# Kernel tuning notes

Measured on AMD Instinct MI355X. Metric: run time of the kernel, lower is better.

## Reference

```python
import jax, jax.numpy as jnp
import numpy as np

B, N, F_IN, F_HID, F_OUT = 16, 1024, 512, 512, 512


def setup_inputs() -> dict:
    key = jax.random.key(0)
    ks = jax.random.split(key, 8)
    return {
        "batch_graph": jax.random.normal(ks[0], (B, N, F_IN), dtype=jnp.float32),
        "adj": jax.random.uniform(ks[1], (B, N, N), dtype=jnp.float32),
        "W1": jax.random.normal(ks[2], (F_IN, F_HID), dtype=jnp.float32) * (1.0 / np.sqrt(F_IN)),
        "b1": jax.random.normal(ks[3], (F_HID,), dtype=jnp.float32) * 0.02,
        "W2": jax.random.normal(ks[4], (F_HID, F_HID), dtype=jnp.float32) * (1.0 / np.sqrt(F_HID)),
        "b2": jax.random.normal(ks[5], (F_HID,), dtype=jnp.float32) * 0.02,
        "W3": jax.random.normal(ks[6], (F_HID, F_OUT), dtype=jnp.float32) * (1.0 / np.sqrt(F_HID)),
        "b3": jax.random.normal(ks[7], (F_OUT,), dtype=jnp.float32) * 0.02,
    }


def _normalize_adj(adj):
    # torch: adj.sum(1) sums over rows -> per-column sums, shape [B, N]
    colsum = jnp.sum(adj, axis=1)
    r = jnp.where(colsum > 0, colsum ** -0.5, 0.0)  # inf -> 0 as in original
    # (adj @ diag(r)).T @ diag(r)  ==  r[:,None] * adj^T * r[None,:]  (per batch)
    return r[:, :, None] * jnp.swapaxes(adj, 1, 2) * r[:, None, :]


def reference(batch_graph, adj, W1, b1, W2, b2, W3, b3):
    # The original builds a dense (B*N)x(B*N) block-diagonal adjacency; the
    # block-diagonal matmul is mathematically a per-graph batched matmul.
    # Dropout is identity in eval mode.
    a = _normalize_adj(adj)  # [B, N, N]

    def layer(x, W, b):
        return jnp.einsum('bij,bjf->bif', a, x @ W) + b

    x = jax.nn.relu(layer(batch_graph, W1, b1))
    x = jax.nn.relu(layer(x, W2, b2))
    return layer(x, W3, b3)  # [B, N, F_OUT]
```

## Files before the change

### kernel.cpp

```cpp
#include <hip/hip_runtime.h>
#include <hip/hip_bf16.h>

typedef __bf16 bf16;
typedef __bf16 bf16x8 __attribute__((ext_vector_type(8)));
typedef float f32x4 __attribute__((ext_vector_type(4)));

#define B_ 16
#define N_ 1024
#define F_ 512

__device__ __forceinline__ float rdv(const void* p, size_t i, int f32) {
  return f32 ? ((const float*)p)[i] : (float)((const bf16*)p)[i];
}

__device__ __forceinline__ void gld16(const bf16* g, bf16* l) {
  __builtin_amdgcn_global_load_lds(
      (const __attribute__((address_space(1))) unsigned int*)g,
      (__attribute__((address_space(3))) unsigned int*)l, 16, 0, 0);
}

__global__ void k_detect(const unsigned* __restrict__ w, int* __restrict__ flag) {
  __shared__ int red[256];
  const int t = threadIdx.x;
  int c = 0;
  for (int i = t; i < 4096; i += 256) c += (((w[i] >> 7) & 0xFFu) >= 130u) ? 1 : 0;
  red[t] = c;
  __syncthreads();
  for (int s = 128; s > 0; s >>= 1) {
    if (t < s) red[t] += red[t + s];
    __syncthreads();
  }
  if (t == 0) flag[0] = (red[0] > 100) ? 1 : 0;
}

__global__ void k_prep(const void* b1, const void* b2, const void* b3,
                       const void* W1, const void* W2, const void* W3,
                       const void* X, const int* __restrict__ flag,
                       float* __restrict__ bc, bf16* __restrict__ Wt,
                       bf16* __restrict__ xc) {
  __shared__ float tile[32][33];
  const int bid = blockIdx.x;
  const int t = threadIdx.x;
  const int f = flag[0];
  if (bid < 6) {
    const int j = bid * 256 + t;
    const void* src = (j < 512) ? b1 : (j < 1024 ? b2 : b3);
    bc[j] = rdv(src, (size_t)(j & 511), f);
  } else if (bid < 774) {
    const int bid2 = bid - 6;
    const int z = bid2 >> 8, ti = bid2 & 255;
    const int f0 = (ti & 15) * 32, k0 = (ti >> 4) * 32;
    const int tx = t & 31, ty = t >> 5;
    const void* W = (z == 0) ? W1 : ((z == 1) ? W2 : W3);
    bf16* dst = Wt + (size_t)z * F_ * F_;
#pragma unroll
    for (int s = 0; s < 4; ++s)
      tile[ty + 8 * s][tx] = rdv(W, (size_t)(k0 + ty + 8 * s) * F_ + f0 + tx, f);
    __syncthreads();
#pragma unroll
    for (int s = 0; s < 4; ++s)
      dst[(size_t)(f0 + ty + 8 * s) * F_ + k0 + tx] = (bf16)tile[tx][ty + 8 * s];
  } else {
    const size_t i4 = ((size_t)(bid - 774) * 256 + t) * 4;
    if (f) {
      f32x4 v = *(const f32x4*)((const float*)X + i4);
      bf16 o[4] = {(bf16)v[0], (bf16)v[1], (bf16)v[2], (bf16)v[3]};
      *(ulong1*)&xc[i4] = *(ulong1*)o;
    } else {
      *(ulong1*)&xc[i4] = *(const ulong1*)((const bf16*)X + i4);
    }
  }
}

__global__ void k_colsum(const void* adj, const int* __restrict__ flag,
                         float* __restrict__ csp) {
  __shared__ float red[256];
  const int t = threadIdx.x;
  const int jj = t & 63, ic = t >> 6;
  const int b = blockIdx.y, z = blockIdx.z;
  const int j0 = blockIdx.x * 64;
  const size_t base = (size_t)b * N_ * N_ + (size_t)(z * 256 + ic * 64) * N_ + j0 + jj;
  float s = 0.f;
  if (flag[0]) {
    const float* p = (const float*)adj + base;
#pragma unroll 16
    for (int i = 0; i < 64; ++i) s += p[(size_t)i * N_];
  } else {
    const bf16* p = (const bf16*)adj + base;
#pragma unroll 16
    for (int i = 0; i < 64; ++i) s += (float)p[(size_t)i * N_];
  }
  red[t] = s;
  __syncthreads();
  if (t < 64)
    csp[((size_t)z * B_ + b) * N_ + j0 + t] = red[t] + red[t + 64] + red[t + 128] + red[t + 192];
}

__device__ __forceinline__ float csum(const float* csp, int b, int j) {
  float c = 0.f;
#pragma unroll
  for (int z = 0; z < 4; ++z) c += csp[((size_t)z * B_ + b) * N_ + j];
  return c;
}

__global__ void k_anorm(const void* adj, const int* __restrict__ flag,
                        const float* __restrict__ csp, bf16* __restrict__ anorm) {
  __shared__ float tile[32][33];
  const int tx = threadIdx.x, ty = threadIdx.y;
  const int f = flag[0];
  const int b = blockIdx.z, i0 = blockIdx.y * 32, j0 = blockIdx.x * 32;
  const size_t sb = (size_t)b * N_ * N_;
#pragma unroll
  for (int s = 0; s < 4; ++s) {
    int jj = ty + 8 * s;
    tile[jj][tx] = rdv(adj, sb + (size_t)(j0 + jj) * N_ + i0 + tx, f);
  }
  float cj = csum(csp, b, j0 + tx);
  float rj = cj > 0.f ? rsqrtf(cj) : 0.f;
  __syncthreads();
  bf16* dst = anorm + sb;
#pragma unroll
  for (int s = 0; s < 4; ++s) {
    int ii = ty + 8 * s;
    float ci = csum(csp, b, i0 + ii);
    float ri = ci > 0.f ? rsqrtf(ci) : 0.f;
    dst[(size_t)(i0 + ii) * N_ + j0 + tx] = (bf16)(ri * tile[tx][ii] * rj);
  }
}

template <int BIAS, int RELU, int OUTDYN>
__global__ __launch_bounds__(256)
void k_gemm_bt(const bf16* __restrict__ A, const bf16* __restrict__ Bt,
               const float* __restrict__ bias, void* __restrict__ C,
               const int* __restrict__ flag,
               int Nc, int K, long sA, long sB, long sC) {
  __shared__ __align__(16) char smem[36864];
  bf16* As = (bf16*)smem;
  bf16* Bs = (bf16*)(smem + 16384);
  const int tid = threadIdx.x;
  const int wid = tid >> 6, lane = tid & 63;
  const int wm = wid >> 1, wn = wid & 1;
  const int quad = lane >> 4, l16 = lane & 15;
  const int rl = lane >> 3;
  const int cg8 = ((lane & 7) ^ rl) * 8;
  const int h = l16 & 7;

  const bf16* gA = A + (size_t)blockIdx.z * sA + (size_t)blockIdx.y * 128 * K;
  const bf16* gB = Bt + (size_t)blockIdx.z * sB + (size_t)blockIdx.x * 128 * K;

  f32x4 acc[4][4];
#pragma unroll
  for (int i = 0; i < 4; ++i)
#pragma unroll
    for (int j = 0; j < 4; ++j) acc[i][j] = (f32x4){0.f, 0.f, 0.f, 0.f};

  for (int k0 = 0; k0 < K; k0 += 64) {
#pragma unroll
    for (int i = 0; i < 4; ++i) {
      const int r0 = wid * 32 + i * 8;
      gld16(gA + (size_t)(r0 + rl) * K + k0 + cg8, &As[r0 * 64]);
      gld16(gB + (size_t)(r0 + rl) * K + k0 + cg8, &Bs[r0 * 64]);
    }
    __syncthreads();

#pragma unroll
    for (int s = 0; s < 2; ++s) {
      bf16x8 af[4], bfv[4];
#pragma unroll
      for (int tm = 0; tm < 4; ++tm)
        af[tm] = *(const bf16x8*)&As[(wm * 64 + tm * 16 + l16) * 64 +
                                     (((quad + 4 * s) ^ h) * 8)];
#pragma unroll
      for (int tn = 0; tn < 4; ++tn)
        bfv[tn] = *(const bf16x8*)&Bs[(wn * 64 + tn * 16 + l16) * 64 +
                                      (((quad + 4 * s) ^ h) * 8)];
#pragma unroll
      for (int tm = 0; tm < 4; ++tm)
#pragma unroll
        for (int tn = 0; tn < 4; ++tn)
          acc[tm][tn] =
              __builtin_amdgcn_mfma_f32_16x16x32_bf16(af[tm], bfv[tn], acc[tm][tn], 0, 0, 0);
    }
    __syncthreads();
  }

  const size_t cb = (size_t)blockIdx.z * sC;
  const int mb_w = blockIdx.y * 128 + wm * 64;
  const int nb_w = blockIdx.x * 128 + wn * 64;

  if (OUTDYN) {
    const int of32 = flag[0];
#pragma unroll
    for (int tn = 0; tn < 4; ++tn) {
      const int n = nb_w + tn * 16 + l16;
      float bv = BIAS ? bias[n] : 0.f;
#pragma unroll
      for (int tm = 0; tm < 4; ++tm) {
        const int m0 = mb_w + tm * 16 + quad * 4;
#pragma unroll
        for (int r = 0; r < 4; ++r) {
          float v = acc[tm][tn][r] + bv;
          if (RELU) v = v > 0.f ? v : 0.f;
          const size_t idx = cb + (size_t)(m0 + r) * Nc + n;
          if (of32) ((float*)C)[idx] = v;
          else      ((bf16*)C)[idx] = (bf16)v;
        }
      }
    }
  } else {
    bf16* W = (bf16*)smem + wid * (64 * 72);
#pragma unroll
    for (int tn = 0; tn < 4; ++tn) {
      const int n = nb_w + tn * 16 + l16;
      float bv = BIAS ? bias[n] : 0.f;
#pragma unroll
      for (int tm = 0; tm < 4; ++tm) {
#pragma unroll
        for (int r = 0; r < 4; ++r) {
          float v = acc[tm][tn][r] + bv;
          if (RELU) v = v > 0.f ? v : 0.f;
          W[(tm * 16 + quad * 4 + r) * 72 + tn * 16 + l16] = (bf16)v;
        }
      }
    }
    bf16* gC = (bf16*)C + cb;
#pragma unroll
    for (int i = 0; i < 8; ++i) {
      const int row = i * 8 + rl;
      bf16x8 v = *(const bf16x8*)&W[row * 72 + (lane & 7) * 8];
      *(bf16x8*)&gC[(size_t)(mb_w + row) * Nc + nb_w + (lane & 7) * 8] = v;
    }
  }
}

extern "C" void kernel_launch(void* const* d_in, const int* in_sizes, int n_in,
                              void* d_out, int out_size, void* d_ws, size_t ws_size,
                              hipStream_t stream) {
  char* ws = (char*)d_ws;
  float* csp  = (float*)ws;
  int*  flag  = (int*)(ws + 262144);
  float* bc   = (float*)(ws + 262400);
  bf16* anorm = (bf16*)(ws + 270592);
  bf16* Wt    = (bf16*)(ws + 270592 + 33554432);
  bf16* Zt    = (bf16*)(ws + 270592 + 33554432 + 3 * F_ * F_ * 2);
  bf16* Xc = (bf16*)d_out;

  const long sW = 0;
  const long sX = (long)N_ * F_;
  const long sZ = (long)F_ * N_;
  const long sAn = (long)N_ * N_;

  k_detect<<<1, 256, 0, stream>>>((const unsigned*)d_in[2], flag);
  k_prep<<<774 + (B_ * N_ * F_) / 1024, 256, 0, stream>>>(
      d_in[3], d_in[5], d_in[7], d_in[2], d_in[4], d_in[6], d_in[0], flag, bc, Wt, Xc);
  k_colsum<<<dim3(N_ / 64, B_, 4), 256, 0, stream>>>(d_in[1], flag, csp);
  k_anorm<<<dim3(N_ / 32, N_ / 32, B_), dim3(32, 8), 0, stream>>>(d_in[1], flag, csp, anorm);

  dim3 g1(N_ / 128, F_ / 128, B_);
  dim3 g2(F_ / 128, N_ / 128, B_);

  k_gemm_bt<0, 0, 0><<<g1, 256, 0, stream>>>(Wt,               Xc, nullptr,   Zt, flag, N_, F_, sW, sX, sZ);
  k_gemm_bt<1, 1, 0><<<g2, 256, 0, stream>>>(anorm,            Zt, bc,        Xc, flag, F_, N_, sAn, sZ, sX);
  k_gemm_bt<0, 0, 0><<<g1, 256, 0, stream>>>(Wt + F_ * F_,     Xc, nullptr,   Zt, flag, N_, F_, sW, sX, sZ);
  k_gemm_bt<1, 1, 0><<<g2, 256, 0, stream>>>(anorm,            Zt, bc + 512,  Xc, flag, F_, N_, sAn, sZ, sX);
  k_gemm_bt<0, 0, 0><<<g1, 256, 0, stream>>>(Wt + 2 * F_ * F_, Xc, nullptr,   Zt, flag, N_, F_, sW, sX, sZ);
  k_gemm_bt<1, 0, 1><<<g2, 256, 0, stream>>>(anorm,            Zt, bc + 1024, d_out, flag, F_, N_, sAn, sZ, sX);
}
```

Measured before the change: 309.6 us.

## Double-buffer GEMM LDS loads and vectorize the adjacency normalize transpose

```diff
diff --git a/kernel.cpp b/kernel.cpp
--- a/kernel.cpp
+++ b/kernel.cpp
@@ -2,6 +2,7 @@
 #include <hip/hip_bf16.h>
 
 typedef __bf16 bf16;
+typedef __bf16 bf16x4 __attribute__((ext_vector_type(4)));
 typedef __bf16 bf16x8 __attribute__((ext_vector_type(8)));
 typedef float f32x4 __attribute__((ext_vector_type(4)));
 
@@ -105,26 +106,49 @@
 
 __global__ void k_anorm(const void* adj, const int* __restrict__ flag,
                         const float* __restrict__ csp, bf16* __restrict__ anorm) {
-  __shared__ float tile[32][33];
+  __shared__ float tile[64][65];
+  __shared__ float rI[64], rJ[64];
   const int tx = threadIdx.x, ty = threadIdx.y;
-  const int f = flag[0];
-  const int b = blockIdx.z, i0 = blockIdx.y * 32, j0 = blockIdx.x * 32;
+  const int t = ty * 16 + tx;
+  const int b = blockIdx.z, i0 = blockIdx.y * 64, j0 = blockIdx.x * 64;
   const size_t sb = (size_t)b * N_ * N_;
-#pragma unroll
-  for (int s = 0; s < 4; ++s) {
-    int jj = ty + 8 * s;
-    tile[jj][tx] = rdv(adj, sb + (size_t)(j0 + jj) * N_ + i0 + tx, f);
-  }
-  float cj = csum(csp, b, j0 + tx);
-  float rj = cj > 0.f ? rsqrtf(cj) : 0.f;
+  if (t < 64) {
+    float c = csum(csp, b, i0 + t);
+    rI[t] = c > 0.f ? rsqrtf(c) : 0.f;
+  } else if (t < 128) {
+    float c = csum(csp, b, j0 + (t - 64));
+    rJ[t - 64] = c > 0.f ? rsqrtf(c) : 0.f;
+  }
+  if (flag[0]) {
+    const float* src = (const float*)adj + sb;
+#pragma unroll
+    for (int s = 0; s < 4; ++s) {
+      const int jj = ty + 16 * s;
+      f32x4 v = *(const f32x4*)&src[(size_t)(j0 + jj) * N_ + i0 + 4 * tx];
+#pragma unroll
+      for (int u = 0; u < 4; ++u) tile[jj][4 * tx + u] = v[u];
+    }
+  } else {
+    const bf16* src = (const bf16*)adj + sb;
+#pragma unroll
+    for (int s = 0; s < 4; ++s) {
+      const int jj = ty + 16 * s;
+      bf16x4 v = *(const bf16x4*)&src[(size_t)(j0 + jj) * N_ + i0 + 4 * tx];
+#pragma unroll
+      for (int u = 0; u < 4; ++u) tile[jj][4 * tx + u] = (float)v[u];
+    }
+  }
   __syncthreads();
   bf16* dst = anorm + sb;
 #pragma unroll
   for (int s = 0; s < 4; ++s) {
-    int ii = ty + 8 * s;
-    float ci = csum(csp, b, i0 + ii);
-    float ri = ci > 0.f ? rsqrtf(ci) : 0.f;
-    dst[(size_t)(i0 + ii) * N_ + j0 + tx] = (bf16)(ri * tile[tx][ii] * rj);
+    const int ii = ty + 16 * s;
+    const float ri = rI[ii];
+    bf16x4 o;
+#pragma unroll
+    for (int u = 0; u < 4; ++u)
+      o[u] = (bf16)(ri * tile[4 * tx + u][ii] * rJ[4 * tx + u]);
+    *(bf16x4*)&dst[(size_t)(i0 + ii) * N_ + j0 + 4 * tx] = o;
   }
 }
 
@@ -134,9 +158,7 @@
                const float* __restrict__ bias, void* __restrict__ C,
                const int* __restrict__ flag,
                int Nc, int K, long sA, long sB, long sC) {
-  __shared__ __align__(16) char smem[36864];
-  bf16* As = (bf16*)smem;
-  bf16* Bs = (bf16*)(smem + 16384);
+  __shared__ __align__(16) char smem[65536];
   const int tid = threadIdx.x;
   const int wid = tid >> 6, lane = tid & 63;
   const int wm = wid >> 1, wn = wid & 1;
@@ -154,15 +176,28 @@
 #pragma unroll
     for (int j = 0; j < 4; ++j) acc[i][j] = (f32x4){0.f, 0.f, 0.f, 0.f};
 
-  for (int k0 = 0; k0 < K; k0 += 64) {
+  auto stage = [&](int d, int k0) {
+    bf16* As = (bf16*)(smem + d * 32768);
+    bf16* Bs = (bf16*)(smem + d * 32768 + 16384);
 #pragma unroll
     for (int i = 0; i < 4; ++i) {
       const int r0 = wid * 32 + i * 8;
       gld16(gA + (size_t)(r0 + rl) * K + k0 + cg8, &As[r0 * 64]);
       gld16(gB + (size_t)(r0 + rl) * K + k0 + cg8, &Bs[r0 * 64]);
     }
-    __syncthreads();
-
+  };
+
+  stage(0, 0);
+  for (int k0 = 0; k0 < K; k0 += 64) {
+    const int cur = (k0 >> 6) & 1;
+    if (k0 + 64 < K) {
+      stage(1 - cur, k0 + 64);
+      asm volatile("s_waitcnt vmcnt(8)\n\ts_barrier" ::: "memory");
+    } else {
+      asm volatile("s_waitcnt vmcnt(0)\n\ts_barrier" ::: "memory");
+    }
+    const bf16* As = (const bf16*)(smem + cur * 32768);
+    const bf16* Bs = (const bf16*)(smem + cur * 32768 + 16384);
 #pragma unroll
     for (int s = 0; s < 2; ++s) {
       bf16x8 af[4], bfv[4];
@@ -181,7 +216,7 @@
           acc[tm][tn] =
               __builtin_amdgcn_mfma_f32_16x16x32_bf16(af[tm], bfv[tn], acc[tm][tn], 0, 0, 0);
     }
-    __syncthreads();
+    asm volatile("s_barrier" ::: "memory");
   }
 
   const size_t cb = (size_t)blockIdx.z * sC;
@@ -254,7 +289,7 @@
   k_prep<<<774 + (B_ * N_ * F_) / 1024, 256, 0, stream>>>(
       d_in[3], d_in[5], d_in[7], d_in[2], d_in[4], d_in[6], d_in[0], flag, bc, Wt, Xc);
   k_colsum<<<dim3(N_ / 64, B_, 4), 256, 0, stream>>>(d_in[1], flag, csp);
-  k_anorm<<<dim3(N_ / 32, N_ / 32, B_), dim3(32, 8), 0, stream>>>(d_in[1], flag, csp, anorm);
+  k_anorm<<<dim3(N_ / 64, N_ / 64, B_), dim3(16, 16), 0, stream>>>(d_in[1], flag, csp, anorm);
 
   dim3 g1(N_ / 128, F_ / 128, B_);
   dim3 g2(F_ / 128, N_ / 128, B_);
```

New measurement: 296.2 us. -4.3%, faster.
